# Performance work log

Measured on AMD Instinct MI355X. Metric: run time of the kernel, lower is better.

The kernel has to match this reference:

```python
import jax, jax.numpy as jnp
import numpy as np

N, TX, NH, H, E, V = 64, 1024, 512, 512, 300, 32000
IP = NH + H            # attention input size = 1024
HALF = IP // 2         # 512
BN_EPS = 1e-5


def setup_inputs() -> dict:
    key = jax.random.key(0)
    ks = jax.random.split(key, 24)
    p = lambda k, shape: jax.random.normal(k, shape, dtype=jnp.float32) * 0.05
    embed_W = p(ks[0], (V, E)).at[0].set(0.0)  # padding_idx=0 row zeroed
    return {
        "yt_prev": jax.random.randint(ks[1], (N,), 0, V, dtype=jnp.int32),
        "h0": jax.random.normal(ks[2], (N, H), dtype=jnp.float32),
        "c0": jax.random.normal(ks[3], (N, H), dtype=jnp.float32),
        "h1": jax.random.normal(ks[4], (N, H), dtype=jnp.float32),
        "c1": jax.random.normal(ks[5], (N, H), dtype=jnp.float32),
        "encoder_output": jax.random.normal(ks[6], (N, TX, NH), dtype=jnp.float32),
        "c_prev": jax.random.normal(ks[7], (N, NH), dtype=jnp.float32),
        "embed_W": embed_W,
        # pre LSTM cell: input = NH + E
        "pre_W_ih": p(ks[8], (4 * H, NH + E)), "pre_W_hh": p(ks[9], (4 * H, H)),
        "pre_b_ih": p(ks[10], (4 * H,)), "pre_b_hh": p(ks[11], (4 * H,)),
        # post LSTM cell: input = H + NH
        "post_W_ih": p(ks[12], (4 * H, H + NH)), "post_W_hh": p(ks[13], (4 * H, H)),
        "post_b_ih": p(ks[14], (4 * H,)), "post_b_hh": p(ks[15], (4 * H,)),
        # attention MLP
        "att_W1": p(ks[16], (HALF, IP)), "att_b1": p(ks[17], (HALF,)),
        "att_W2": p(ks[18], (1, HALF)), "att_b2": p(ks[19], (1,)),
        # classifier
        "mlp_W": p(ks[20], (V, H)), "mlp_b": p(ks[21], (V,)),
        "bn_gamma": jnp.ones((V,), jnp.float32), "bn_beta": jnp.zeros((V,), jnp.float32),
    }


def _lstm_cell(x, h, c, W_ih, W_hh, b_ih, b_hh):
    # PyTorch LSTMCell gate order: i, f, g, o
    g = x @ W_ih.T + h @ W_hh.T + (b_ih + b_hh)
    i, f, gg, o = jnp.split(g, 4, axis=-1)
    c_new = jax.nn.sigmoid(f) * c + jax.nn.sigmoid(i) * jnp.tanh(gg)
    h_new = jax.nn.sigmoid(o) * jnp.tanh(c_new)
    return h_new, c_new


def reference(yt_prev, h0, c0, h1, c1, encoder_output, c_prev, embed_W,
              pre_W_ih, pre_W_hh, pre_b_ih, pre_b_hh,
              post_W_ih, post_W_hh, post_b_ih, post_b_hh,
              att_W1, att_b1, att_W2, att_b2,
              mlp_W, mlp_b, bn_gamma, bn_beta):
    # embedding lookup + concat with previous context
    y_emb = embed_W[yt_prev]                              # [N, E]
    rnn_input = jnp.concatenate([y_emb, c_prev], axis=1)  # [N, E+NH]
    h_0, c_0 = _lstm_cell(rnn_input, h0, c0, pre_W_ih, pre_W_hh, pre_b_ih, pre_b_hh)
    s_i = h_0
    # Bahdanau attention over encoder timesteps
    Tx = encoder_output.shape[1]
    s_exp = jnp.broadcast_to(s_i[:, None, :], (s_i.shape[0], Tx, s_i.shape[1]))
    concat = jnp.concatenate([encoder_output, s_exp], axis=2)  # [N, Tx, IP]
    e = jax.nn.relu(concat @ att_W1.T + att_b1)                # [N, Tx, HALF]
    scores = e @ att_W2.T + att_b2                             # [N, Tx, 1]
    alphas = jax.nn.softmax(scores, axis=1)                    # softmax over Tx
    context = jnp.sum(alphas * encoder_output, axis=1)         # [N, NH]
    # post LSTM cell
    spell_input = jnp.concatenate([s_i, context], axis=1)
    h_1, c_1 = _lstm_cell(spell_input, h1, c1, post_W_ih, post_W_hh, post_b_ih, post_b_hh)
    # classifier: linear -> relu -> batchnorm(train mode, batch stats) -> softmax
    z = jax.nn.relu(h_1 @ mlp_W.T + mlp_b)                     # [N, V]
    mean = jnp.mean(z, axis=0)
    var = jnp.mean((z - mean) ** 2, axis=0)                    # biased, as in PyTorch training
    z_bn = bn_gamma * (z - mean) * jax.lax.rsqrt(var + BN_EPS) + bn_beta
    out = jax.nn.softmax(z_bn, axis=1)
    return out, h_0, c_0, h_1, c_1, context
```

## Files before the change

kernel.cpp:

```cpp
#include <hip/hip_runtime.h>
#include <math.h>

#define DEVFN __device__ __forceinline__

typedef __attribute__((ext_vector_type(4))) float f32x4;
typedef __attribute__((ext_vector_type(8))) __bf16 bf16x8;
typedef __attribute__((ext_vector_type(8))) short short8v;

#define NB   64
#define TXD  1024
#define NHD  512
#define HSZ  512
#define ESZ  300
#define VSZ  32000
#define G4   (4*HSZ)
#define KPRE (ESZ + NHD + HSZ)
#define KPOST 1536
#define HALFD 512

DEVFN short f2bf(float f) {
  unsigned u = __float_as_uint(f);
  u = (u + 0x7fffu + ((u >> 16) & 1u)) >> 16;
  return (short)u;
}
DEVFN float sigm(float x) { return 1.0f / (1.0f + __expf(-x)); }

DEVFN short8v pack8(float4 a, float4 b) {
  short8v v;
  v[0]=f2bf(a.x); v[1]=f2bf(a.y); v[2]=f2bf(a.z); v[3]=f2bf(a.w);
  v[4]=f2bf(b.x); v[5]=f2bf(b.y); v[6]=f2bf(b.z); v[7]=f2bf(b.w);
  return v;
}
DEVFN void gload16(const void* g, void* lds_base) {
  __builtin_amdgcn_global_load_lds(
      (const __attribute__((address_space(1))) unsigned int*)g,
      (__attribute__((address_space(3))) unsigned int*)lds_base, 16, 0, 0);
}

DEVFN float4 ldA4(const float* __restrict__ A, int lda, int row, int k, int Ka) {
  if (k >= Ka) { float4 z = {0.f,0.f,0.f,0.f}; return z; }
  return *(const float4*)(A + (size_t)row * lda + k);
}
DEVFN float4 ldB4(const float* __restrict__ B1, int ldb1, int split,
                  const float* __restrict__ B2, int ldb2, int row, int k, int Ka) {
  if (k >= Ka) { float4 z = {0.f,0.f,0.f,0.f}; return z; }
  if (k < split) return *(const float4*)(B1 + (size_t)row * ldb1 + k);
  return *(const float4*)(B2 + (size_t)row * ldb2 + (k - split));
}

__global__ __launch_bounds__(256)
void prep(const int* __restrict__ yt, const float* __restrict__ embW,
          const float* __restrict__ c_prev, const float* __restrict__ h0,
          const float* __restrict__ W1, unsigned short* __restrict__ W1b,
          float* __restrict__ cat)
{
  int b = blockIdx.x;
  if (b < 128) {
    int i = b * 256 + threadIdx.x;
    int c = i >> 6, kq = (i & 63) * 8;
    float4 a = *(const float4*)(W1 + (size_t)c * 1024 + kq);
    float4 bb = *(const float4*)(W1 + (size_t)c * 1024 + kq + 4);
    *(short8v*)(W1b + (size_t)c * 512 + kq) = pack8(a, bb);
  } else {
    int i = (b - 128) * 256 + threadIdx.x;
    if (i >= NB * KPRE) return;
    int n = i / KPRE, c = i - n * KPRE;
    float v;
    if (c < ESZ)            v = embW[(size_t)yt[n] * ESZ + c];
    else if (c < ESZ + NHD) v = c_prev[(size_t)n * NHD + (c - ESZ)];
    else                    v = h0[(size_t)n * HSZ + (c - ESZ - NHD)];
    cat[i] = v;
  }
}

template<int EPI>
__global__ __launch_bounds__(256)
void mfma_gemm128(const float* __restrict__ A, int lda, int Ka,
                  const float* __restrict__ B1, int ldb1, int split,
                  const float* __restrict__ B2, int ldb2,
                  const float* __restrict__ bias1,
                  float* __restrict__ C, int ldc, int Kslice,
                  const float* __restrict__ gamma, const float* __restrict__ beta,
                  float* __restrict__ bnsc, float* __restrict__ bnsh)
{
  __shared__ __align__(16) short As[64][40];
  __shared__ __align__(16) short Bs[128][40];
  const int tid = threadIdx.x;
  const int w = tid >> 6, lane = tid & 63;
  const int wr = w >> 1, wc = w & 1;
  const int cl = lane & 15, g = lane >> 4;
  const int n0 = blockIdx.x * 128;
  const int ks = blockIdx.y;
  const int kbeg = ks * Kslice;
  const int kend = min(kbeg + Kslice, Ka);
  C += (size_t)ks * 64 * ldc;

  const f32x4 fz = {0.f,0.f,0.f,0.f};
  f32x4 acc[2][4];
  #pragma unroll
  for (int i = 0; i < 2; ++i)
    #pragma unroll
    for (int j = 0; j < 4; ++j) acc[i][j] = fz;

  const int sr  = tid >> 2;
  const int skc = (tid & 3) * 8;

  float4 ra0, ra1, rb0[2], rb1[2];
  ra0 = ldA4(A, lda, sr, kbeg + skc, Ka);
  ra1 = ldA4(A, lda, sr, kbeg + skc + 4, Ka);
  #pragma unroll
  for (int it = 0; it < 2; ++it) {
    rb0[it] = ldB4(B1, ldb1, split, B2, ldb2, n0 + sr + it*64, kbeg + skc, Ka);
    rb1[it] = ldB4(B1, ldb1, split, B2, ldb2, n0 + sr + it*64, kbeg + skc + 4, Ka);
  }

  for (int k0 = kbeg; k0 < kend; k0 += 32) {
    __syncthreads();
    *(short8v*)&As[sr][skc] = pack8(ra0, ra1);
    #pragma unroll
    for (int it = 0; it < 2; ++it)
      *(short8v*)&Bs[sr + it*64][skc] = pack8(rb0[it], rb1[it]);
    __syncthreads();
    if (k0 + 32 < kend) {
      ra0 = ldA4(A, lda, sr, k0 + 32 + skc, Ka);
      ra1 = ldA4(A, lda, sr, k0 + 32 + skc + 4, Ka);
      #pragma unroll
      for (int it = 0; it < 2; ++it) {
        rb0[it] = ldB4(B1, ldb1, split, B2, ldb2, n0 + sr + it*64, k0 + 32 + skc, Ka);
        rb1[it] = ldB4(B1, ldb1, split, B2, ldb2, n0 + sr + it*64, k0 + 32 + skc + 4, Ka);
      }
    }
    bf16x8 af[2], bfr[4];
    #pragma unroll
    for (int mi = 0; mi < 2; ++mi)
      af[mi] = *(const bf16x8*)&As[wr*32 + mi*16 + cl][g * 8];
    #pragma unroll
    for (int ni = 0; ni < 4; ++ni)
      bfr[ni] = *(const bf16x8*)&Bs[wc*64 + ni*16 + cl][g * 8];
    #pragma unroll
    for (int mi = 0; mi < 2; ++mi)
      #pragma unroll
      for (int ni = 0; ni < 4; ++ni)
        acc[mi][ni] = __builtin_amdgcn_mfma_f32_16x16x32_bf16(af[mi], bfr[ni], acc[mi][ni], 0, 0, 0);
  }

  float s1[4] = {0.f,0.f,0.f,0.f}, s2[4] = {0.f,0.f,0.f,0.f};
  #pragma unroll
  for (int ni = 0; ni < 4; ++ni) {
    int nn = n0 + wc*64 + ni*16 + cl;
    float b = (EPI == 4) ? bias1[nn] : 0.f;
    #pragma unroll
    for (int mi = 0; mi < 2; ++mi)
      #pragma unroll
      for (int r = 0; r < 4; ++r) {
        int m = wr*32 + mi*16 + g*4 + r;
        float v = acc[mi][ni][r];
        if (EPI == 4) v = fmaxf(v + b, 0.f);
        C[(size_t)m * ldc + nn] = v;
        if (EPI == 4) { s1[ni] += v; s2[ni] = fmaf(v, v, s2[ni]); }
      }
  }
  if (EPI == 4) {
    #pragma unroll
    for (int mm = 16; mm < 64; mm <<= 1)
      #pragma unroll
      for (int ni = 0; ni < 4; ++ni) {
        s1[ni] += __shfl_xor(s1[ni], mm, 64);
        s2[ni] += __shfl_xor(s2[ni], mm, 64);
      }
    float* red = (float*)As;
    __syncthreads();
    if (g == 0) {
      #pragma unroll
      for (int ni = 0; ni < 4; ++ni) {
        int col = wc*64 + ni*16 + cl;
        red[(wr*128 + col)*2 + 0] = s1[ni];
        red[(wr*128 + col)*2 + 1] = s2[ni];
      }
    }
    __syncthreads();
    if (tid < 128) {
      int col = n0 + tid;
      float a1 = red[tid*2] + red[(128 + tid)*2];
      float a2 = red[tid*2 + 1] + red[(128 + tid)*2 + 1];
      float mean = a1 * (1.0f / NB);
      float var = a2 * (1.0f / NB) - mean * mean;
      float rr = rsqrtf(var + 1e-5f);
      float sc = gamma[col] * rr;
      bnsc[col] = sc;
      bnsh[col] = beta[col] - mean * sc;
    }
  }
}

__global__ __launch_bounds__(256)
void lstm_point2(const float* __restrict__ gp, int np,
                 const float* __restrict__ bih, const float* __restrict__ bhh,
                 const float* __restrict__ c_old,
                 float* __restrict__ h_new, float* __restrict__ c_new)
{
  int i = blockIdx.x * 256 + threadIdx.x;
  int n = i >> 9, k = i & 511;
  float g[4];
  #pragma unroll
  for (int j = 0; j < 4; ++j) {
    int idx = j * 512 + k;
    float s = bih[idx] + bhh[idx];
    for (int ks = 0; ks < np; ++ks)
      s += gp[((size_t)ks*64 + n) * G4 + idx];
    g[j] = s;
  }
  float c = sigm(g[1]) * c_old[i] + sigm(g[0]) * tanhf(g[2]);
  float h = sigm(g[3]) * tanhf(c);
  h_new[i] = h; c_new[i] = c;
}

__global__ __launch_bounds__(256)
void att_score(const float* __restrict__ enc, const unsigned short* __restrict__ W1b,
               const float* __restrict__ W2, const float* __restrict__ sprojp,
               const float* __restrict__ b1, float* __restrict__ spart)
{
  __shared__ __align__(16) char smem[40960];
  const int tid = threadIdx.x;
  const int wid = tid >> 6, lane = tid & 63;
  const int cl = lane & 15, g = lane >> 4;
  const int rt = blockIdx.x >> 1, ch = blockIdx.x & 1;
  const int r0 = rt << 6;
  const int c0 = ch << 8;
  const int n  = rt >> 4;

  const int a_row = ((tid >> 3) << 1) + ((tid >> 2) & 1);
  const int a_qf  = (((tid & 3) ^ ((tid >> 3) & 3)) << 3);
  const int b_r = ((lane >> 3) << 1) + ((lane >> 2) & 1);
  const int b_q = (((lane & 3) ^ ((lane >> 3) & 3)) << 3);

  const f32x4 fz = {0.f,0.f,0.f,0.f};
  f32x4 acc[4][4];
  #pragma unroll
  for (int mi = 0; mi < 4; ++mi)
    #pragma unroll
    for (int ni = 0; ni < 4; ++ni) acc[mi][ni] = fz;

  float4 a_lo, a_hi;
  #define A_LOAD(tt) do { \
    const float* asrc = enc + (size_t)(r0 + a_row) * 512 + (tt) * 32 + a_qf; \
    a_lo = *(const float4*)asrc; a_hi = *(const float4*)(asrc + 4); } while (0)
  #define A_WRITE(buf) \
    *(short8v*)(smem + (buf) * 4096 + tid * 16) = pack8(a_lo, a_hi)
  #define STAGE_B(buf, tt) do { int k0 = (tt) * 32; \
    _Pragma("unroll") \
    for (int jj = 0; jj < 4; ++jj) { int j = (wid << 2) + jj; \
      gload16(W1b + (size_t)(c0 + (j << 4) + b_r) * 512 + k0 + b_q, \
              smem + 8192 + (buf) * 16384 + (j << 10)); } } while (0)

  A_LOAD(0);
  STAGE_B(0, 0);
  asm volatile("s_waitcnt vmcnt(4)" ::: "memory");
  A_WRITE(0);
  A_LOAD(1);
  asm volatile("s_waitcnt vmcnt(2)" ::: "memory");
  asm volatile("s_waitcnt lgkmcnt(0)" ::: "memory");
  __builtin_amdgcn_s_barrier();
  __builtin_amdgcn_sched_barrier(0);

  for (int t = 0; t < 16; ++t) {
    const int s = t & 1;
    if (t < 15) {
      STAGE_B(s ^ 1, t + 1);
      asm volatile("s_waitcnt vmcnt(4)" ::: "memory");
      A_WRITE(s ^ 1);
      if (t < 14) A_LOAD(t + 2);
    }
    const char* Ab = smem + s * 4096;
    const char* Bb = smem + 8192 + s * 16384;
    bf16x8 af[4];
    #pragma unroll
    for (int mi = 0; mi < 4; ++mi) {
      int r = mi * 16 + cl;
      af[mi] = *(const bf16x8*)(Ab + (r >> 1) * 128 + (r & 1) * 64
                                + ((g ^ ((r >> 1) & 3)) << 4));
    }
    #pragma unroll
    for (int ni = 0; ni < 4; ++ni) {
      int r = wid * 64 + ni * 16 + cl;
      bf16x8 bf = *(const bf16x8*)(Bb + (r >> 1) * 128 + (r & 1) * 64
                                   + ((g ^ ((r >> 1) & 3)) << 4));
      #pragma unroll
      for (int mi = 0; mi < 4; ++mi)
        acc[mi][ni] = __builtin_amdgcn_mfma_f32_16x16x32_bf16(af[mi], bf, acc[mi][ni], 0, 0, 0);
    }
    if (t < 15) {
      if (t < 14) asm volatile("s_waitcnt vmcnt(2)" ::: "memory");
      else        asm volatile("s_waitcnt vmcnt(0)" ::: "memory");
      asm volatile("s_waitcnt lgkmcnt(0)" ::: "memory");
      __builtin_amdgcn_s_barrier();
      __builtin_amdgcn_sched_barrier(0);
    }
  }
  #undef A_LOAD
  #undef A_WRITE
  #undef STAGE_B
  __syncthreads();

  float part[4][4] = {};
  #pragma unroll
  for (int ni = 0; ni < 4; ++ni) {
    int c = c0 + wid*64 + ni*16 + cl;
    float spv = b1[c];
    #pragma unroll
    for (int ks = 0; ks < 4; ++ks)
      spv += sprojp[((size_t)ks*64 + n) * HALFD + c];
    float w2 = W2[c];
    #pragma unroll
    for (int mi = 0; mi < 4; ++mi)
      #pragma unroll
      for (int r = 0; r < 4; ++r)
        part[mi][r] += fmaxf(acc[mi][ni][r] + spv, 0.f) * w2;
  }
  #pragma unroll
  for (int mm = 1; mm < 16; mm <<= 1)
    #pragma unroll
    for (int mi = 0; mi < 4; ++mi)
      #pragma unroll
      for (int r = 0; r < 4; ++r)
        part[mi][r] += __shfl_xor(part[mi][r], mm, 64);
  float* red = (float*)smem;
  if (cl == 0) {
    #pragma unroll
    for (int mi = 0; mi < 4; ++mi)
      #pragma unroll
      for (int r = 0; r < 4; ++r)
        red[wid*64 + mi*16 + g*4 + r] = part[mi][r];
  }
  __syncthreads();
  if (tid < 64)
    spart[(size_t)ch * (NB*TXD) + r0 + tid] =
        red[tid] + red[64 + tid] + red[128 + tid] + red[192 + tid];
}

__global__ __launch_bounds__(256)
void softmax_tx(const float* __restrict__ spart, float* __restrict__ alphas)
{
  int n = blockIdx.x, tid = threadIdx.x;
  __shared__ float rb[4];
  __shared__ float sb[4];
  float v[4]; float mx = -1e30f;
  #pragma unroll
  for (int i = 0; i < 4; ++i) {
    int t = tid + i*256;
    v[i] = spart[(size_t)n*TXD + t] + spart[(size_t)NB*TXD + (size_t)n*TXD + t];
    mx = fmaxf(mx, v[i]);
  }
  #pragma unroll
  for (int m = 32; m >= 1; m >>= 1) mx = fmaxf(mx, __shfl_xor(mx, m, 64));
  if ((tid & 63) == 0) rb[tid >> 6] = mx;
  __syncthreads();
  mx = fmaxf(fmaxf(rb[0], rb[1]), fmaxf(rb[2], rb[3]));
  float s = 0.f;
  #pragma unroll
  for (int i = 0; i < 4; ++i) { v[i] = __expf(v[i] - mx); s += v[i]; }
  #pragma unroll
  for (int m = 32; m >= 1; m >>= 1) s += __shfl_xor(s, m, 64);
  if ((tid & 63) == 0) sb[tid >> 6] = s;
  __syncthreads();
  s = sb[0] + sb[1] + sb[2] + sb[3];
  float inv = 1.0f / s;
  #pragma unroll
  for (int i = 0; i < 4; ++i) alphas[(size_t)n*TXD + tid + i*256] = v[i] * inv;
}

__global__ __launch_bounds__(512)
void context_partial(const float* __restrict__ enc, const float* __restrict__ alphas,
                     float* __restrict__ part)
{
  int n = blockIdx.y, chunk = blockIdx.x;
  int c = threadIdx.x;
  __shared__ float al[128];
  if (threadIdx.x < 128) al[threadIdx.x] = alphas[(size_t)n*TXD + chunk*128 + threadIdx.x];
  __syncthreads();
  const float* e = enc + ((size_t)n*TXD + chunk*128) * NHD + c;
  float s = 0.f;
  #pragma unroll 4
  for (int t = 0; t < 128; ++t) s = fmaf(al[t], e[(size_t)t * NHD], s);
  part[((size_t)n*8 + chunk) * NHD + c] = s;
}

__global__ __launch_bounds__(256)
void finalize_context(const float* __restrict__ part, const float* __restrict__ h0out,
                      const float* __restrict__ h1in,
                      float* __restrict__ ctx_out, float* __restrict__ cat)
{
  int i = blockIdx.x * 256 + threadIdx.x;
  int n = i >> 9, c = i & 511;
  float s = 0.f;
  #pragma unroll
  for (int j = 0; j < 8; ++j) s += part[((size_t)n*8 + j) * NHD + c];
  ctx_out[i] = s;
  cat[(size_t)n * KPOST + c] = h0out[i];
  cat[(size_t)n * KPOST + HSZ + c] = s;
  cat[(size_t)n * KPOST + 2*HSZ + c] = h1in[i];
}

__global__ __launch_bounds__(1024)
void softmax_v(const float* __restrict__ z, const float* __restrict__ scale,
               const float* __restrict__ shift, float* __restrict__ out)
{
  int n = blockIdx.x, tid = threadIdx.x;
  const float* zr = z + (size_t)n * VSZ;
  float* orow = out + (size_t)n * VSZ;
  __shared__ float rb[16];
  __shared__ float sb[16];
  float v[32]; float mx = -1e30f;
  #pragma unroll
  for (int i = 0; i < 32; ++i) {
    int j = tid + i*1024;
    v[i] = (j < VSZ) ? fmaf(zr[j], scale[j], shift[j]) : -1e30f;
    mx = fmaxf(mx, v[i]);
  }
  #pragma unroll
  for (int m = 32; m >= 1; m >>= 1) mx = fmaxf(mx, __shfl_xor(mx, m, 64));
  if ((tid & 63) == 0) rb[tid >> 6] = mx;
  __syncthreads();
  #pragma unroll
  for (int i = 0; i < 16; ++i) mx = fmaxf(mx, rb[i]);
  float s = 0.f;
  #pragma unroll
  for (int i = 0; i < 32; ++i) { v[i] = __expf(v[i] - mx); s += v[i]; }
  #pragma unroll
  for (int m = 32; m >= 1; m >>= 1) s += __shfl_xor(s, m, 64);
  if ((tid & 63) == 0) sb[tid >> 6] = s;
  __syncthreads();
  s = 0.f;
  #pragma unroll
  for (int i = 0; i < 16; ++i) s += sb[i];
  float inv = 1.0f / s;
  #pragma unroll
  for (int i = 0; i < 32; ++i) {
    int j = tid + i*1024;
    if (j < VSZ) orow[j] = v[i] * inv;
  }
}

extern "C" void kernel_launch(void* const* d_in, const int* in_sizes, int n_in,
                              void* d_out, int out_size, void* d_ws, size_t ws_size,
                              hipStream_t stream)
{
  const int*   yt       = (const int*)  d_in[0];
  const float* h0       = (const float*)d_in[1];
  const float* c0       = (const float*)d_in[2];
  const float* h1       = (const float*)d_in[3];
  const float* c1       = (const float*)d_in[4];
  const float* enc      = (const float*)d_in[5];
  const float* c_prev   = (const float*)d_in[6];
  const float* embW     = (const float*)d_in[7];
  const float* pre_Wih  = (const float*)d_in[8];
  const float* pre_Whh  = (const float*)d_in[9];
  const float* pre_bih  = (const float*)d_in[10];
  const float* pre_bhh  = (const float*)d_in[11];
  const float* post_Wih = (const float*)d_in[12];
  const float* post_Whh = (const float*)d_in[13];
  const float* post_bih = (const float*)d_in[14];
  const float* post_bhh = (const float*)d_in[15];
  const float* att_W1   = (const float*)d_in[16];
  const float* att_b1   = (const float*)d_in[17];
  const float* att_W2   = (const float*)d_in[18];
  const float* mlp_W    = (const float*)d_in[20];
  const float* mlp_b    = (const float*)d_in[21];
  const float* bn_g     = (const float*)d_in[22];
  const float* bn_b     = (const float*)d_in[23];

  float* out   = (float*)d_out;
  float* o_h0  = out + (size_t)NB * VSZ;
  float* o_c0  = o_h0 + NB * HSZ;
  float* o_h1  = o_c0 + NB * HSZ;
  float* o_c1  = o_h1 + NB * HSZ;
  float* o_ctx = o_c1 + NB * HSZ;

  float* ws = (float*)d_ws;
  float* pre_cat  = ws;
  float* gatesp   = ws + 84736;
  float* sprojp   = ws + 1264384;
  float* spart    = ws + 1395456;
  float* alphas   = ws + 1526528;
  float* ctxp     = ws + 1592064;
  float* post_cat = ws + 1854208;
  unsigned short* W1b = (unsigned short*)(ws + 1952512);
  float* zbuf     = ws;
  float* bnsc     = ws + 2083584;
  float* bnsh     = ws + 2115584;

  prep<<<459, 256, 0, stream>>>(yt, embW, c_prev, h0, att_W1, W1b, pre_cat);
  mfma_gemm128<0><<<dim3(G4/128, 9), 256, 0, stream>>>(
      pre_cat, KPRE, KPRE, pre_Wih, ESZ + NHD, ESZ + NHD, pre_Whh, HSZ,
      nullptr, gatesp, G4, 160, nullptr, nullptr, nullptr, nullptr);
  lstm_point2<<<NB*HSZ/256, 256, 0, stream>>>(gatesp, 9, pre_bih, pre_bhh, c0, o_h0, o_c0);
  mfma_gemm128<0><<<dim3(HALFD/128, 4), 256, 0, stream>>>(
      o_h0, HSZ, HSZ, att_W1 + NHD, NHD + HSZ, HSZ, att_W1 + NHD, NHD + HSZ,
      nullptr, sprojp, HALFD, 128, nullptr, nullptr, nullptr, nullptr);
  att_score<<<2048, 256, 0, stream>>>(enc, W1b, att_W2, sprojp, att_b1, spart);
  softmax_tx<<<NB, 256, 0, stream>>>(spart, alphas);
  context_partial<<<dim3(8, NB), 512, 0, stream>>>(enc, alphas, ctxp);
  finalize_context<<<NB*NHD/256, 256, 0, stream>>>(ctxp, o_h0, h1, o_ctx, post_cat);
  mfma_gemm128<0><<<dim3(G4/128, 8), 256, 0, stream>>>(
      post_cat, KPOST, KPOST, post_Wih, HSZ + NHD, HSZ + NHD, post_Whh, HSZ,
      nullptr, gatesp, G4, 192, nullptr, nullptr, nullptr, nullptr);
  lstm_point2<<<NB*HSZ/256, 256, 0, stream>>>(gatesp, 8, post_bih, post_bhh, c1, o_h1, o_c1);
  mfma_gemm128<4><<<dim3(VSZ/128, 1), 256, 0, stream>>>(
      o_h1, HSZ, HSZ, mlp_W, HSZ, HSZ, mlp_W, HSZ, mlp_b, zbuf, VSZ, 512,
      bn_g, bn_b, bnsc, bnsh);
  softmax_v<<<NB, 1024, 0, stream>>>(zbuf, bnsc, bnsh, out);
}
```

Before: 170.9 us.

## Fuse attention scoring, tile softmax, and context accumulation into one kernel

The attention score kernel now covers all 512 hidden columns per 64-row tile, so it no longer splits columns across two blocks. It also computes a tile-local softmax (max and sum of exponentials) and the exp-weighted context partial while the encoder tile is still cache-hot. A small combine kernel merges the 16 per-tile partials per batch row using online-softmax rescaling, which replaces the separate softmax_tx, context_partial and finalize_context kernels and the alphas round trip. In exchange, shared memory grows to 72KB, accumulators double to 4x8, and the hand-tuned waitcnt pipeline is replaced by plain __syncthreads, which may lower occupancy and load/compute overlap.

```diff
diff --git a/kernel.cpp b/kernel.cpp
--- a/kernel.cpp
+++ b/kernel.cpp
@@ -216,63 +216,55 @@
 }
 
 __global__ __launch_bounds__(256)
-void att_score(const float* __restrict__ enc, const unsigned short* __restrict__ W1b,
+void att_fused(const float* __restrict__ enc, const unsigned short* __restrict__ W1b,
                const float* __restrict__ W2, const float* __restrict__ sprojp,
-               const float* __restrict__ b1, float* __restrict__ spart)
-{
-  __shared__ __align__(16) char smem[40960];
+               const float* __restrict__ b1,
+               float* __restrict__ mbuf, float* __restrict__ sbuf,
+               float* __restrict__ ctxp)
+{
+  __shared__ __align__(16) char smem[73728];
   const int tid = threadIdx.x;
   const int wid = tid >> 6, lane = tid & 63;
   const int cl = lane & 15, g = lane >> 4;
-  const int rt = blockIdx.x >> 1, ch = blockIdx.x & 1;
+  const int rt = blockIdx.x;
   const int r0 = rt << 6;
-  const int c0 = ch << 8;
   const int n  = rt >> 4;
 
-  const int a_row = ((tid >> 3) << 1) + ((tid >> 2) & 1);
-  const int a_qf  = (((tid & 3) ^ ((tid >> 3) & 3)) << 3);
+  const int a_row = tid >> 2;
+  const int a_line = a_row >> 1;
+  const int a_waddr = a_line*128 + (a_row & 1)*64 + (((tid & 3) ^ (a_line & 3)) << 4);
   const int b_r = ((lane >> 3) << 1) + ((lane >> 2) & 1);
   const int b_q = (((lane & 3) ^ ((lane >> 3) & 3)) << 3);
 
   const f32x4 fz = {0.f,0.f,0.f,0.f};
-  f32x4 acc[4][4];
+  f32x4 acc[4][8];
   #pragma unroll
   for (int mi = 0; mi < 4; ++mi)
     #pragma unroll
-    for (int ni = 0; ni < 4; ++ni) acc[mi][ni] = fz;
+    for (int ni = 0; ni < 8; ++ni) acc[mi][ni] = fz;
 
   float4 a_lo, a_hi;
   #define A_LOAD(tt) do { \
-    const float* asrc = enc + (size_t)(r0 + a_row) * 512 + (tt) * 32 + a_qf; \
+    const float* asrc = enc + (size_t)(r0 + a_row) * 512 + (tt) * 32 + (tid & 3) * 8; \
     a_lo = *(const float4*)asrc; a_hi = *(const float4*)(asrc + 4); } while (0)
   #define A_WRITE(buf) \
-    *(short8v*)(smem + (buf) * 4096 + tid * 16) = pack8(a_lo, a_hi)
+    *(short8v*)(smem + (buf) * 4096 + a_waddr) = pack8(a_lo, a_hi)
   #define STAGE_B(buf, tt) do { int k0 = (tt) * 32; \
     _Pragma("unroll") \
-    for (int jj = 0; jj < 4; ++jj) { int j = (wid << 2) + jj; \
-      gload16(W1b + (size_t)(c0 + (j << 4) + b_r) * 512 + k0 + b_q, \
-              smem + 8192 + (buf) * 16384 + (j << 10)); } } while (0)
+    for (int jj = 0; jj < 8; ++jj) { int j = (wid << 3) + jj; \
+      gload16(W1b + (size_t)((j << 4) + b_r) * 512 + k0 + b_q, \
+              smem + 8192 + (buf) * 32768 + (j << 10)); } } while (0)
 
   A_LOAD(0);
   STAGE_B(0, 0);
-  asm volatile("s_waitcnt vmcnt(4)" ::: "memory");
   A_WRITE(0);
-  A_LOAD(1);
-  asm volatile("s_waitcnt vmcnt(2)" ::: "memory");
-  asm volatile("s_waitcnt lgkmcnt(0)" ::: "memory");
-  __builtin_amdgcn_s_barrier();
-  __builtin_amdgcn_sched_barrier(0);
+  __syncthreads();
 
   for (int t = 0; t < 16; ++t) {
     const int s = t & 1;
-    if (t < 15) {
-      STAGE_B(s ^ 1, t + 1);
-      asm volatile("s_waitcnt vmcnt(4)" ::: "memory");
-      A_WRITE(s ^ 1);
-      if (t < 14) A_LOAD(t + 2);
-    }
+    if (t < 15) { A_LOAD(t + 1); STAGE_B(s ^ 1, t + 1); }
     const char* Ab = smem + s * 4096;
-    const char* Bb = smem + 8192 + s * 16384;
+    const char* Bb = smem + 8192 + s * 32768;
     bf16x8 af[4];
     #pragma unroll
     for (int mi = 0; mi < 4; ++mi) {
@@ -281,31 +273,25 @@
                                 + ((g ^ ((r >> 1) & 3)) << 4));
     }
     #pragma unroll
-    for (int ni = 0; ni < 4; ++ni) {
-      int r = wid * 64 + ni * 16 + cl;
+    for (int ni = 0; ni < 8; ++ni) {
+      int r = wid * 128 + ni * 16 + cl;
       bf16x8 bf = *(const bf16x8*)(Bb + (r >> 1) * 128 + (r & 1) * 64
                                    + ((g ^ ((r >> 1) & 3)) << 4));
       #pragma unroll
       for (int mi = 0; mi < 4; ++mi)
         acc[mi][ni] = __builtin_amdgcn_mfma_f32_16x16x32_bf16(af[mi], bf, acc[mi][ni], 0, 0, 0);
     }
-    if (t < 15) {
-      if (t < 14) asm volatile("s_waitcnt vmcnt(2)" ::: "memory");
-      else        asm volatile("s_waitcnt vmcnt(0)" ::: "memory");
-      asm volatile("s_waitcnt lgkmcnt(0)" ::: "memory");
-      __builtin_amdgcn_s_barrier();
-      __builtin_amdgcn_sched_barrier(0);
-    }
+    if (t < 15) A_WRITE(s ^ 1);
+    __syncthreads();
   }
   #undef A_LOAD
   #undef A_WRITE
   #undef STAGE_B
-  __syncthreads();
 
   float part[4][4] = {};
   #pragma unroll
-  for (int ni = 0; ni < 4; ++ni) {
-    int c = c0 + wid*64 + ni*16 + cl;
+  for (int ni = 0; ni < 8; ++ni) {
+    int c = wid*128 + ni*16 + cl;
     float spv = b1[c];
     #pragma unroll
     for (int ks = 0; ks < 4; ++ks)
@@ -325,6 +311,8 @@
       for (int r = 0; r < 4; ++r)
         part[mi][r] += __shfl_xor(part[mi][r], mm, 64);
   float* red = (float*)smem;
+  float* sc  = (float*)(smem + 4096);
+  float* eV  = (float*)(smem + 4352);
   if (cl == 0) {
     #pragma unroll
     for (int mi = 0; mi < 4; ++mi)
@@ -333,71 +321,71 @@
         red[wid*64 + mi*16 + g*4 + r] = part[mi][r];
   }
   __syncthreads();
-  if (tid < 64)
-    spart[(size_t)ch * (NB*TXD) + r0 + tid] =
-        red[tid] + red[64 + tid] + red[128 + tid] + red[192 + tid];
+  if (tid < 64) {
+    float s = red[tid] + red[64 + tid] + red[128 + tid] + red[192 + tid];
+    sc[tid] = s;
+    float M = s;
+    #pragma unroll
+    for (int mm = 32; mm >= 1; mm >>= 1) M = fmaxf(M, __shfl_xor(M, mm, 64));
+    float e = __expf(s - M);
+    eV[tid] = e;
+    float S = e;
+    #pragma unroll
+    for (int mm = 32; mm >= 1; mm >>= 1) S += __shfl_xor(S, mm, 64);
+    if (tid == 0) { mbuf[rt] = M; sbuf[rt] = S; }
+  }
+  __syncthreads();
+
+  f32x4* red4 = (f32x4*)(smem + 8192);
+  {
+    const int cgrp = tid & 127, tq = tid >> 7;
+    const float* ebase = enc + (size_t)r0 * 512 + (cgrp << 2);
+    f32x4 a4 = fz;
+    #pragma unroll 8
+    for (int tt = 0; tt < 32; ++tt) {
+      int t = tq*32 + tt;
+      float et = eV[t];
+      float4 x = *(const float4*)(ebase + (size_t)t * 512);
+      a4[0] = fmaf(et, x.x, a4[0]);
+      a4[1] = fmaf(et, x.y, a4[1]);
+      a4[2] = fmaf(et, x.z, a4[2]);
+      a4[3] = fmaf(et, x.w, a4[3]);
+    }
+    red4[tq*128 + cgrp] = a4;
+  }
+  __syncthreads();
+  if (tid < 128) {
+    f32x4 s4 = red4[tid];
+    f32x4 b4 = red4[128 + tid];
+    f32x4 o4;
+    #pragma unroll
+    for (int i = 0; i < 4; ++i) o4[i] = s4[i] + b4[i];
+    *(f32x4*)(ctxp + (size_t)rt * 512 + tid*4) = o4;
+  }
 }
 
 __global__ __launch_bounds__(256)
-void softmax_tx(const float* __restrict__ spart, float* __restrict__ alphas)
-{
-  int n = blockIdx.x, tid = threadIdx.x;
-  __shared__ float rb[4];
-  __shared__ float sb[4];
-  float v[4]; float mx = -1e30f;
-  #pragma unroll
-  for (int i = 0; i < 4; ++i) {
-    int t = tid + i*256;
-    v[i] = spart[(size_t)n*TXD + t] + spart[(size_t)NB*TXD + (size_t)n*TXD + t];
-    mx = fmaxf(mx, v[i]);
-  }
-  #pragma unroll
-  for (int m = 32; m >= 1; m >>= 1) mx = fmaxf(mx, __shfl_xor(mx, m, 64));
-  if ((tid & 63) == 0) rb[tid >> 6] = mx;
-  __syncthreads();
-  mx = fmaxf(fmaxf(rb[0], rb[1]), fmaxf(rb[2], rb[3]));
-  float s = 0.f;
-  #pragma unroll
-  for (int i = 0; i < 4; ++i) { v[i] = __expf(v[i] - mx); s += v[i]; }
-  #pragma unroll
-  for (int m = 32; m >= 1; m >>= 1) s += __shfl_xor(s, m, 64);
-  if ((tid & 63) == 0) sb[tid >> 6] = s;
-  __syncthreads();
-  s = sb[0] + sb[1] + sb[2] + sb[3];
-  float inv = 1.0f / s;
-  #pragma unroll
-  for (int i = 0; i < 4; ++i) alphas[(size_t)n*TXD + tid + i*256] = v[i] * inv;
-}
-
-__global__ __launch_bounds__(512)
-void context_partial(const float* __restrict__ enc, const float* __restrict__ alphas,
-                     float* __restrict__ part)
-{
-  int n = blockIdx.y, chunk = blockIdx.x;
-  int c = threadIdx.x;
-  __shared__ float al[128];
-  if (threadIdx.x < 128) al[threadIdx.x] = alphas[(size_t)n*TXD + chunk*128 + threadIdx.x];
-  __syncthreads();
-  const float* e = enc + ((size_t)n*TXD + chunk*128) * NHD + c;
-  float s = 0.f;
-  #pragma unroll 4
-  for (int t = 0; t < 128; ++t) s = fmaf(al[t], e[(size_t)t * NHD], s);
-  part[((size_t)n*8 + chunk) * NHD + c] = s;
-}
-
-__global__ __launch_bounds__(256)
-void finalize_context(const float* __restrict__ part, const float* __restrict__ h0out,
-                      const float* __restrict__ h1in,
-                      float* __restrict__ ctx_out, float* __restrict__ cat)
+void att_combine(const float* __restrict__ mbuf, const float* __restrict__ sbuf,
+                 const float* __restrict__ ctxp, const float* __restrict__ h0out,
+                 const float* __restrict__ h1in,
+                 float* __restrict__ ctx_out, float* __restrict__ cat)
 {
   int i = blockIdx.x * 256 + threadIdx.x;
   int n = i >> 9, c = i & 511;
-  float s = 0.f;
-  #pragma unroll
-  for (int j = 0; j < 8; ++j) s += part[((size_t)n*8 + j) * NHD + c];
-  ctx_out[i] = s;
+  float M = -1e30f;
+  #pragma unroll
+  for (int b = 0; b < 16; ++b) M = fmaxf(M, mbuf[n*16 + b]);
+  float S = 0.f, ctx = 0.f;
+  #pragma unroll
+  for (int b = 0; b < 16; ++b) {
+    float w = __expf(mbuf[n*16 + b] - M);
+    S = fmaf(sbuf[n*16 + b], w, S);
+    ctx = fmaf(ctxp[(size_t)(n*16 + b)*512 + c], w, ctx);
+  }
+  ctx /= S;
+  ctx_out[i] = ctx;
   cat[(size_t)n * KPOST + c] = h0out[i];
-  cat[(size_t)n * KPOST + HSZ + c] = s;
+  cat[(size_t)n * KPOST + HSZ + c] = ctx;
   cat[(size_t)n * KPOST + 2*HSZ + c] = h1in[i];
 }
 
@@ -480,14 +468,14 @@
   float* pre_cat  = ws;
   float* gatesp   = ws + 84736;
   float* sprojp   = ws + 1264384;
-  float* spart    = ws + 1395456;
-  float* alphas   = ws + 1526528;
-  float* ctxp     = ws + 1592064;
-  float* post_cat = ws + 1854208;
-  unsigned short* W1b = (unsigned short*)(ws + 1952512);
+  float* mbuf     = ws + 1395456;
+  float* sbuf     = ws + 1396480;
+  float* ctxp     = ws + 1397504;
+  float* post_cat = ws + 1921792;
+  unsigned short* W1b = (unsigned short*)(ws + 2020096);
   float* zbuf     = ws;
-  float* bnsc     = ws + 2083584;
-  float* bnsh     = ws + 2115584;
+  float* bnsc     = ws + 2151168;
+  float* bnsh     = ws + 2183168;
 
   prep<<<459, 256, 0, stream>>>(yt, embW, c_prev, h0, att_W1, W1b, pre_cat);
   mfma_gemm128<0><<<dim3(G4/128, 9), 256, 0, stream>>>(
@@ -497,10 +485,9 @@
   mfma_gemm128<0><<<dim3(HALFD/128, 4), 256, 0, stream>>>(
       o_h0, HSZ, HSZ, att_W1 + NHD, NHD + HSZ, HSZ, att_W1 + NHD, NHD + HSZ,
       nullptr, sprojp, HALFD, 128, nullptr, nullptr, nullptr, nullptr);
-  att_score<<<2048, 256, 0, stream>>>(enc, W1b, att_W2, sprojp, att_b1, spart);
-  softmax_tx<<<NB, 256, 0, stream>>>(spart, alphas);
-  context_partial<<<dim3(8, NB), 512, 0, stream>>>(enc, alphas, ctxp);
-  finalize_context<<<NB*NHD/256, 256, 0, stream>>>(ctxp, o_h0, h1, o_ctx, post_cat);
+  att_fused<<<1024, 256, 0, stream>>>(enc, W1b, att_W2, sprojp, att_b1,
+                                      mbuf, sbuf, ctxp);
+  att_combine<<<NB*NHD/256, 256, 0, stream>>>(mbuf, sbuf, ctxp, o_h0, h1, o_ctx, post_cat);
   mfma_gemm128<0><<<dim3(G4/128, 8), 256, 0, stream>>>(
       post_cat, KPOST, KPOST, post_Wih, HSZ + NHD, HSZ + NHD, post_Whh, HSZ,
       nullptr, gatesp, G4, 192, nullptr, nullptr, nullptr, nullptr);
```

Result: slower. 183.7 us (+7.5%).
